# Kernel optimization log

Measured on AMD Instinct MI355X. Metric: run time of the kernel, lower is better.

The kernel has to match this reference:

```python
import jax, jax.numpy as jnp
import numpy as np

B, L, H = 8, 4096, 1024
S = 32            # sentences (sep tokens) per sample, fixed for stackability
SEP_ID = 102      # BERT [SEP]
NUM_LABELS = 2
LN_EPS = 1e-5


def _make_ids_and_mask():
    rng = np.random.default_rng(0)
    ids = rng.integers(1000, 30000, size=(B, L))
    for i in range(B):
        pos = np.sort(rng.choice(np.arange(1, L), size=S, replace=False))
        ids[i, pos] = SEP_ID
    mask = np.ones((B, L), dtype=np.int32)
    return jnp.asarray(ids, dtype=jnp.int64), jnp.asarray(mask)


def setup_inputs() -> dict:
    key = jax.random.key(0)
    ks = jax.random.split(key, 4)
    input_ids, attention_mask = _make_ids_and_mask()
    std = 0.02
    return {
        "seq": jax.random.normal(ks[0], (B, L, H), dtype=jnp.float32),
        "input_ids": input_ids,
        "attention_mask": attention_mask,
        "W1": jax.random.normal(ks[1], (H, H), dtype=jnp.float32) * std,
        "b1": jnp.zeros((H,), jnp.float32),
        "ln_g": jnp.ones((H,), jnp.float32),
        "ln_b": jnp.zeros((H,), jnp.float32),
        "W2": jax.random.normal(ks[2], (H, NUM_LABELS), dtype=jnp.float32) * std,
        "b2": jnp.zeros((NUM_LABELS,), jnp.float32),
    }


def _segment_means(seq, input_ids, attention_mask):
    # sep positions per sample, fixed count S -> [B, S]
    sep_pos = jax.vmap(
        lambda ids: jnp.nonzero(ids == SEP_ID, size=S, fill_value=L - 1)[0]
    )(input_ids)
    bounds = jnp.concatenate(
        [jnp.zeros((seq.shape[0], 1), sep_pos.dtype), sep_pos], axis=1
    )  # [B, S+1]
    st, ed = bounds[:, :-1], bounds[:, 1:]  # inclusive span [st, ed]

    m = attention_mask.astype(seq.dtype)[..., None]            # [B,L,1]
    # exclusive prefix sums -> sum over [st, ed] = P[ed+1] - P[st]
    P = jnp.pad(jnp.cumsum(seq * m, axis=1), ((0, 0), (1, 0), (0, 0)))   # [B,L+1,H]
    C = jnp.pad(jnp.cumsum(attention_mask.astype(jnp.int32), axis=1), ((0, 0), (1, 0)))

    sums = (jnp.take_along_axis(P, (ed + 1)[..., None], axis=1)
            - jnp.take_along_axis(P, st[..., None], axis=1))   # [B,S,H]
    cnts = (jnp.take_along_axis(C, ed + 1, axis=1)
            - jnp.take_along_axis(C, st, axis=1))              # [B,S]
    cnts = jnp.maximum(cnts, 1).astype(seq.dtype)
    return sums / cnts[..., None]


def reference(seq, input_ids, attention_mask, W1, b1, ln_g, ln_b, W2, b2):
    reps = _segment_means(seq, input_ids, attention_mask)      # [B,S,H]
    h = jnp.einsum("bsh,hk->bsk", reps, W1) + b1
    mu = jnp.mean(h, axis=-1, keepdims=True)
    var = jnp.var(h, axis=-1, keepdims=True)
    h = (h - mu) * jax.lax.rsqrt(var + LN_EPS) * ln_g + ln_b
    h = jax.nn.gelu(h, approximate=False)   # torch nn.GELU default (erf); dropout is eval-mode identity
    return jnp.einsum("bsk,kn->bsn", h, W2) + b2               # [B,S,num_labels]
```

## Files before the change

kernel.cpp:

```cpp
#include <hip/hip_runtime.h>
#include <math.h>

#define BB 8
#define LL 4096
#define HH 1024
#define SS 32
#define SEPID 102
#define NROWS 256
#define TOK 64
#define SPLITK 8
#define KSLICE (HH / SPLITK)

__global__ __launch_bounds__(256) void prep_kernel(
    const int* __restrict__ ids, const int* __restrict__ mask,
    float* __restrict__ cnts, int* __restrict__ spos_g) {
  int b = blockIdx.x;
  int tid = threadIdx.x;
  __shared__ int spos_raw[SS];
  __shared__ int spos[SS];
  __shared__ int nsep;
  __shared__ int excl_s[257];
  __shared__ int wtot[4];
  if (tid == 0) nsep = 0;
  if (tid < SS) spos_raw[tid] = LL - 1;
  __syncthreads();
  const int* idb = ids + (size_t)b * LL;
  const int* mb  = mask + (size_t)b * LL;

  for (int t = tid; t < LL; t += 256) {
    if (idb[t] == SEPID) {
      int slot = atomicAdd(&nsep, 1);
      if (slot < SS) spos_raw[slot] = t;
    }
  }
  __syncthreads();
  if (tid < SS) {
    int p = spos_raw[tid];
    int rank = 0;
    for (int j = 0; j < SS; j++) {
      int q = spos_raw[j];
      rank += (q < p) || (q == p && j < tid);
    }
    spos[rank] = p;
  }

  int local = 0;
  int base = tid * 16;
#pragma unroll
  for (int i = 0; i < 16; i++) local += mb[base + i];
  int lane = tid & 63, wave = tid >> 6;
  int v = local;
#pragma unroll
  for (int off = 1; off < 64; off <<= 1) {
    int n = __shfl_up(v, off, 64);
    if (lane >= off) v += n;
  }
  if (lane == 63) wtot[wave] = v;
  __syncthreads();
  int woff = 0;
  for (int w = 0; w < wave; w++) woff += wtot[w];
  excl_s[tid] = woff + v - local;
  if (tid == 0) excl_s[256] = wtot[0] + wtot[1] + wtot[2] + wtot[3];
  __syncthreads();

  if (tid < SS) {
    spos_g[b * SS + tid] = spos[tid];
    int st = (tid == 0) ? 0 : spos[tid - 1];
    int ed = spos[tid];
    int pa = st, pb = ed + 1;
    int ca = excl_s[pa >> 4];
    for (int i = pa & ~15; i < pa; i++) ca += mb[i];
    int cb = excl_s[pb >> 4];
    for (int i = pb & ~15; i < pb; i++) cb += mb[i];
    cnts[b * SS + tid] = (float)max(cb - ca, 1);
  }
}

__device__ __forceinline__ void flush_seg(float* __restrict__ sums, int b,
                                          int seg, int tid, const float4& acc) {
  if (seg >= 0) {
    float* p = sums + ((size_t)(b * SS + seg)) * HH + tid * 4;
    atomicAdd(p + 0, acc.x);
    atomicAdd(p + 1, acc.y);
    atomicAdd(p + 2, acc.z);
    atomicAdd(p + 3, acc.w);
  }
}

__global__ __launch_bounds__(256) void segsum_kernel(
    const float4* __restrict__ seq, const int* __restrict__ mask,
    const int* __restrict__ spos_g, float* __restrict__ sums) {
  const int chunks = LL / TOK;
  int b = blockIdx.x / chunks;
  int c = blockIdx.x % chunks;
  int t0 = c * TOK;
  int tid = threadIdx.x;
  __shared__ int sposs[SS];
  __shared__ int scode[TOK];
  if (tid < SS) sposs[tid] = spos_g[b * SS + tid];
  __syncthreads();
  if (tid < TOK) {
    int t = t0 + tid;
    int lo = 0, hi = SS;
    while (lo < hi) {
      int mid = (lo + hi) >> 1;
      if (sposs[mid] < t) lo = mid + 1; else hi = mid;
    }
    int issep = (lo < SS && sposs[lo] == t) ? 1 : 0;
    int r = lo;
    int m = mask[(size_t)b * LL + t];
    int live = (issep || r < SS) ? 1 : 0;
    scode[tid] = ((r << 1) | issep) | ((m && live) ? 0x100 : 0);
  }
  __syncthreads();
  float4 acc = make_float4(0.f, 0.f, 0.f, 0.f);
  int curseg = -1;
  const float4* rowbase = seq + (size_t)(b * LL + t0) * (HH / 4) + tid;
  for (int i = 0; i < TOK; i++) {
    float4 v = rowbase[(size_t)i * (HH / 4)];
    int cd = scode[i];
    int r = (cd >> 1) & 0x3F;
    int issep = cd & 1;
    float mf = (cd & 0x100) ? 1.f : 0.f;
    v.x *= mf; v.y *= mf; v.z *= mf; v.w *= mf;
    if (issep) {
      if (curseg != r) {
        flush_seg(sums, b, curseg, tid, acc);
        acc = make_float4(0.f, 0.f, 0.f, 0.f);
      }
      acc.x += v.x; acc.y += v.y; acc.z += v.z; acc.w += v.w;
      flush_seg(sums, b, r, tid, acc);
      if (r + 1 < SS) { curseg = r + 1; acc = v; }
      else { curseg = -1; acc = make_float4(0.f, 0.f, 0.f, 0.f); }
    } else {
      int sg = (r < SS) ? r : -1;
      if (sg != curseg) {
        flush_seg(sums, b, curseg, tid, acc);
        curseg = sg;
        acc = make_float4(0.f, 0.f, 0.f, 0.f);
      }
      acc.x += v.x; acc.y += v.y; acc.z += v.z; acc.w += v.w;
    }
  }
  flush_seg(sums, b, curseg, tid, acc);
}

__global__ __launch_bounds__(256) void gemm1_kernel(
    const float* __restrict__ sums, const float* __restrict__ cnts,
    const float* __restrict__ W1, float* __restrict__ h1p) {
  __shared__ float As[32][68];
  __shared__ float Bs[32][68];
  __shared__ float inv[64];
  int bj = blockIdx.x;
  int bi = blockIdx.y;
  int bz = blockIdx.z;
  int tid = threadIdx.x;
  int r0 = bi * 64, c0 = bj * 64, kb = bz * KSLICE;
  if (tid < 64) inv[tid] = 1.0f / cnts[r0 + tid];

  int ai = tid >> 3;
  int af = tid & 7;
  int bk = tid >> 4;
  int bj4 = tid & 15;
  int tx = tid & 15, ty = tid >> 4;

  float acc[4][4];
#pragma unroll
  for (int i = 0; i < 4; i++)
#pragma unroll
    for (int j = 0; j < 4; j++) acc[i][j] = 0.f;

  for (int k0 = kb; k0 < kb + KSLICE; k0 += 32) {
    __syncthreads();
    float4 a0 = *(const float4*)&sums[(size_t)(r0 + ai) * HH + k0 + af * 4];
    float4 a1 = *(const float4*)&sums[(size_t)(r0 + ai + 32) * HH + k0 + af * 4];
    float4 b0 = *(const float4*)&W1[(size_t)(k0 + bk) * HH + c0 + bj4 * 4];
    float4 b1 = *(const float4*)&W1[(size_t)(k0 + bk + 16) * HH + c0 + bj4 * 4];
    float i0 = inv[ai], i1 = inv[ai + 32];
    As[af * 4 + 0][ai] = a0.x * i0;
    As[af * 4 + 1][ai] = a0.y * i0;
    As[af * 4 + 2][ai] = a0.z * i0;
    As[af * 4 + 3][ai] = a0.w * i0;
    As[af * 4 + 0][ai + 32] = a1.x * i1;
    As[af * 4 + 1][ai + 32] = a1.y * i1;
    As[af * 4 + 2][ai + 32] = a1.z * i1;
    As[af * 4 + 3][ai + 32] = a1.w * i1;
    *(float4*)&Bs[bk][bj4 * 4] = b0;
    *(float4*)&Bs[bk + 16][bj4 * 4] = b1;
    __syncthreads();
#pragma unroll
    for (int kk = 0; kk < 32; kk++) {
      float4 a = *(const float4*)&As[kk][ty * 4];
      float4 b = *(const float4*)&Bs[kk][tx * 4];
      acc[0][0] += a.x * b.x; acc[0][1] += a.x * b.y;
      acc[0][2] += a.x * b.z; acc[0][3] += a.x * b.w;
      acc[1][0] += a.y * b.x; acc[1][1] += a.y * b.y;
      acc[1][2] += a.y * b.z; acc[1][3] += a.y * b.w;
      acc[2][0] += a.z * b.x; acc[2][1] += a.z * b.y;
      acc[2][2] += a.z * b.z; acc[2][3] += a.z * b.w;
      acc[3][0] += a.w * b.x; acc[3][1] += a.w * b.y;
      acc[3][2] += a.w * b.z; acc[3][3] += a.w * b.w;
    }
  }
#pragma unroll
  for (int dr = 0; dr < 4; dr++) {
    float4 o = make_float4(acc[dr][0], acc[dr][1], acc[dr][2], acc[dr][3]);
    *(float4*)&h1p[((size_t)bz * NROWS + r0 + ty * 4 + dr) * HH + c0 + tx * 4] = o;
  }
}

__global__ __launch_bounds__(256) void final_kernel(
    const float* __restrict__ h1p, const float* __restrict__ b1,
    const float* __restrict__ ln_g, const float* __restrict__ ln_b,
    const float* __restrict__ W2, const float* __restrict__ b2,
    float* __restrict__ out) {
  int r = blockIdx.x;
  int tid = threadIdx.x;
  float4 x = ((const float4*)b1)[tid];
#pragma unroll
  for (int sl = 0; sl < SPLITK; sl++) {
    float4 p = ((const float4*)(h1p + ((size_t)sl * NROWS + r) * HH))[tid];
    x.x += p.x; x.y += p.y; x.z += p.z; x.w += p.w;
  }
  float s = x.x + x.y + x.z + x.w;
  float sq = x.x * x.x + x.y * x.y + x.z * x.z + x.w * x.w;
  __shared__ float redA[4], redB[4];
#pragma unroll
  for (int off = 32; off >= 1; off >>= 1) {
    s += __shfl_down(s, off, 64);
    sq += __shfl_down(sq, off, 64);
  }
  int wave = tid >> 6, lane = tid & 63;
  if (lane == 0) { redA[wave] = s; redB[wave] = sq; }
  __syncthreads();
  float ts = redA[0] + redA[1] + redA[2] + redA[3];
  float tq = redB[0] + redB[1] + redB[2] + redB[3];
  float mean = ts * (1.0f / HH);
  float var = tq * (1.0f / HH) - mean * mean;
  float rinv = rsqrtf(var + 1e-5f);
  float4 g4 = ((const float4*)ln_g)[tid];
  float4 bb4 = ((const float4*)ln_b)[tid];
  float4 w20 = ((const float4*)W2)[tid * 2];
  float4 w21 = ((const float4*)W2)[tid * 2 + 1];
  float xs[4] = {x.x, x.y, x.z, x.w};
  float gs[4] = {g4.x, g4.y, g4.z, g4.w};
  float bs[4] = {bb4.x, bb4.y, bb4.z, bb4.w};
  float w0[4] = {w20.x, w20.z, w21.x, w21.z};
  float w1[4] = {w20.y, w20.w, w21.y, w21.w};
  float o0 = 0.f, o1 = 0.f;
#pragma unroll
  for (int j = 0; j < 4; j++) {
    float y = (xs[j] - mean) * rinv * gs[j] + bs[j];
    float gel = 0.5f * y * (1.0f + erff(y * 0.70710678118654752440f));
    o0 += gel * w0[j];
    o1 += gel * w1[j];
  }
#pragma unroll
  for (int off = 32; off >= 1; off >>= 1) {
    o0 += __shfl_down(o0, off, 64);
    o1 += __shfl_down(o1, off, 64);
  }
  __syncthreads();
  if (lane == 0) { redA[wave] = o0; redB[wave] = o1; }
  __syncthreads();
  if (tid == 0) {
    out[(size_t)r * 2 + 0] = redA[0] + redA[1] + redA[2] + redA[3] + b2[0];
    out[(size_t)r * 2 + 1] = redB[0] + redB[1] + redB[2] + redB[3] + b2[1];
  }
}

extern "C" void kernel_launch(void* const* d_in, const int* in_sizes, int n_in,
                              void* d_out, int out_size, void* d_ws, size_t ws_size,
                              hipStream_t stream) {
  (void)in_sizes; (void)n_in; (void)out_size; (void)ws_size;
  const float* seq  = (const float*)d_in[0];
  const int*   ids  = (const int*)d_in[1];
  const int*   mask = (const int*)d_in[2];
  const float* W1   = (const float*)d_in[3];
  const float* b1   = (const float*)d_in[4];
  const float* ln_g = (const float*)d_in[5];
  const float* ln_b = (const float*)d_in[6];
  const float* W2   = (const float*)d_in[7];
  const float* b2   = (const float*)d_in[8];
  float* out = (float*)d_out;

  char* ws = (char*)d_ws;
  float* sums = (float*)ws;
  float* h1p  = (float*)(ws + (1 << 20));
  float* cnts = (float*)(ws + (9 << 20));
  int*   spos = (int*)(ws + (9 << 20) + 4096);

  hipMemsetAsync(sums, 0, (size_t)NROWS * HH * sizeof(float), stream);
  prep_kernel<<<BB, 256, 0, stream>>>(ids, mask, cnts, spos);
  segsum_kernel<<<BB * (LL / TOK), 256, 0, stream>>>(
      (const float4*)seq, mask, spos, sums);
  dim3 g1(16, 4, SPLITK);
  gemm1_kernel<<<g1, 256, 0, stream>>>(sums, cnts, W1, h1p);
  final_kernel<<<NROWS, 256, 0, stream>>>(h1p, b1, ln_g, ln_b, W2, b2, out);
}
```

Measured before the change: 243.2 us.

## Fold memset into prep, skip post-last-sep chunks, prefetch rows, defer mean scaling

Zeroing of the sums buffer moves into extra blocks of the prep kernel, which removes the separate memset launch. Segsum blocks whose token chunk lies entirely after the last separator now exit early, skipping reads of seq rows that belong to no segment. The row loop software-prefetches the next row. Division by segment counts moves from the GEMM's A-tile load into the final kernel, applied once per row after the split-K reduction, and the first barrier in the GEMM loop is dropped. The early exit is exact only because no span extends past the last separator; the 32 separators are random, so the number of tokens it skips is data-dependent.

```diff
diff --git a/kernel.cpp b/kernel.cpp
--- a/kernel.cpp
+++ b/kernel.cpp
@@ -13,9 +13,19 @@
 
 __global__ __launch_bounds__(256) void prep_kernel(
     const int* __restrict__ ids, const int* __restrict__ mask,
-    float* __restrict__ cnts, int* __restrict__ spos_g) {
+    float* __restrict__ cnts, int* __restrict__ spos_g,
+    float* __restrict__ sums) {
   int b = blockIdx.x;
+  int by = blockIdx.y;
   int tid = threadIdx.x;
+  if (by > 0) {
+    int z = b * 8 + (by - 1);
+    float4 zero = make_float4(0.f, 0.f, 0.f, 0.f);
+    float4* p = (float4*)sums + (size_t)z * 1024;
+#pragma unroll
+    for (int i = 0; i < 4; i++) p[tid + i * 256] = zero;
+    return;
+  }
   __shared__ int spos_raw[SS];
   __shared__ int spos[SS];
   __shared__ int nsep;
@@ -99,6 +109,7 @@
   __shared__ int scode[TOK];
   if (tid < SS) sposs[tid] = spos_g[b * SS + tid];
   __syncthreads();
+  if (t0 > sposs[SS - 1]) return;
   if (tid < TOK) {
     int t = t0 + tid;
     int lo = 0, hi = SS;
@@ -115,13 +126,17 @@
   __syncthreads();
   float4 acc = make_float4(0.f, 0.f, 0.f, 0.f);
   int curseg = -1;
-  const float4* rowbase = seq + (size_t)(b * LL + t0) * (HH / 4) + tid;
+  const int rs = HH / 4;
+  const float4* rowbase = seq + (size_t)(b * LL + t0) * rs + tid;
+  float4 vcur = rowbase[0];
   for (int i = 0; i < TOK; i++) {
-    float4 v = rowbase[(size_t)i * (HH / 4)];
+    int nx = (i + 1 < TOK) ? (i + 1) : (TOK - 1);
+    float4 vnext = rowbase[(size_t)nx * rs];
     int cd = scode[i];
     int r = (cd >> 1) & 0x3F;
     int issep = cd & 1;
     float mf = (cd & 0x100) ? 1.f : 0.f;
+    float4 v = vcur;
     v.x *= mf; v.y *= mf; v.z *= mf; v.w *= mf;
     if (issep) {
       if (curseg != r) {
@@ -141,22 +156,21 @@
       }
       acc.x += v.x; acc.y += v.y; acc.z += v.z; acc.w += v.w;
     }
+    vcur = vnext;
   }
   flush_seg(sums, b, curseg, tid, acc);
 }
 
 __global__ __launch_bounds__(256) void gemm1_kernel(
-    const float* __restrict__ sums, const float* __restrict__ cnts,
-    const float* __restrict__ W1, float* __restrict__ h1p) {
+    const float* __restrict__ sums, const float* __restrict__ W1,
+    float* __restrict__ h1p) {
   __shared__ float As[32][68];
   __shared__ float Bs[32][68];
-  __shared__ float inv[64];
   int bj = blockIdx.x;
   int bi = blockIdx.y;
   int bz = blockIdx.z;
   int tid = threadIdx.x;
   int r0 = bi * 64, c0 = bj * 64, kb = bz * KSLICE;
-  if (tid < 64) inv[tid] = 1.0f / cnts[r0 + tid];
 
   int ai = tid >> 3;
   int af = tid & 7;
@@ -171,20 +185,19 @@
     for (int j = 0; j < 4; j++) acc[i][j] = 0.f;
 
   for (int k0 = kb; k0 < kb + KSLICE; k0 += 32) {
-    __syncthreads();
+    if (k0 != kb) __syncthreads();
     float4 a0 = *(const float4*)&sums[(size_t)(r0 + ai) * HH + k0 + af * 4];
     float4 a1 = *(const float4*)&sums[(size_t)(r0 + ai + 32) * HH + k0 + af * 4];
     float4 b0 = *(const float4*)&W1[(size_t)(k0 + bk) * HH + c0 + bj4 * 4];
     float4 b1 = *(const float4*)&W1[(size_t)(k0 + bk + 16) * HH + c0 + bj4 * 4];
-    float i0 = inv[ai], i1 = inv[ai + 32];
-    As[af * 4 + 0][ai] = a0.x * i0;
-    As[af * 4 + 1][ai] = a0.y * i0;
-    As[af * 4 + 2][ai] = a0.z * i0;
-    As[af * 4 + 3][ai] = a0.w * i0;
-    As[af * 4 + 0][ai + 32] = a1.x * i1;
-    As[af * 4 + 1][ai + 32] = a1.y * i1;
-    As[af * 4 + 2][ai + 32] = a1.z * i1;
-    As[af * 4 + 3][ai + 32] = a1.w * i1;
+    As[af * 4 + 0][ai] = a0.x;
+    As[af * 4 + 1][ai] = a0.y;
+    As[af * 4 + 2][ai] = a0.z;
+    As[af * 4 + 3][ai] = a0.w;
+    As[af * 4 + 0][ai + 32] = a1.x;
+    As[af * 4 + 1][ai + 32] = a1.y;
+    As[af * 4 + 2][ai + 32] = a1.z;
+    As[af * 4 + 3][ai + 32] = a1.w;
     *(float4*)&Bs[bk][bj4 * 4] = b0;
     *(float4*)&Bs[bk + 16][bj4 * 4] = b1;
     __syncthreads();
@@ -210,18 +223,24 @@
 }
 
 __global__ __launch_bounds__(256) void final_kernel(
-    const float* __restrict__ h1p, const float* __restrict__ b1,
-    const float* __restrict__ ln_g, const float* __restrict__ ln_b,
-    const float* __restrict__ W2, const float* __restrict__ b2,
-    float* __restrict__ out) {
+    const float* __restrict__ h1p, const float* __restrict__ cnts,
+    const float* __restrict__ b1, const float* __restrict__ ln_g,
+    const float* __restrict__ ln_b, const float* __restrict__ W2,
+    const float* __restrict__ b2, float* __restrict__ out) {
   int r = blockIdx.x;
   int tid = threadIdx.x;
-  float4 x = ((const float4*)b1)[tid];
+  float4 x = make_float4(0.f, 0.f, 0.f, 0.f);
 #pragma unroll
   for (int sl = 0; sl < SPLITK; sl++) {
     float4 p = ((const float4*)(h1p + ((size_t)sl * NROWS + r) * HH))[tid];
     x.x += p.x; x.y += p.y; x.z += p.z; x.w += p.w;
   }
+  float invr = 1.0f / cnts[r];
+  float4 bb1 = ((const float4*)b1)[tid];
+  x.x = x.x * invr + bb1.x;
+  x.y = x.y * invr + bb1.y;
+  x.z = x.z * invr + bb1.z;
+  x.w = x.w * invr + bb1.w;
   float s = x.x + x.y + x.z + x.w;
   float sq = x.x * x.x + x.y * x.y + x.z * x.z + x.w * x.w;
   __shared__ float redA[4], redB[4];
@@ -290,11 +309,11 @@
   float* cnts = (float*)(ws + (9 << 20));
   int*   spos = (int*)(ws + (9 << 20) + 4096);
 
-  hipMemsetAsync(sums, 0, (size_t)NROWS * HH * sizeof(float), stream);
-  prep_kernel<<<BB, 256, 0, stream>>>(ids, mask, cnts, spos);
+  dim3 gp(BB, 9);
+  prep_kernel<<<gp, 256, 0, stream>>>(ids, mask, cnts, spos, sums);
   segsum_kernel<<<BB * (LL / TOK), 256, 0, stream>>>(
       (const float4*)seq, mask, spos, sums);
   dim3 g1(16, 4, SPLITK);
-  gemm1_kernel<<<g1, 256, 0, stream>>>(sums, cnts, W1, h1p);
-  final_kernel<<<NROWS, 256, 0, stream>>>(h1p, b1, ln_g, ln_b, W2, b2, out);
-}
+  gemm1_kernel<<<g1, 256, 0, stream>>>(sums, W1, h1p);
+  final_kernel<<<NROWS, 256, 0, stream>>>(h1p, cnts, b1, ln_g, ln_b, W2, b2, out);
+}
```

Measured after the change: 239.9 us. About the same (-1.4%).
